# Optimization experiments

Hardware: AMD Instinct MI355X
Metric: run time of the kernel (lower is better)

The kernel has to match this reference:

```python
import jax, jax.numpy as jnp
import numpy as np

LAMBDA_TSA = 0.1
K = 25
P = 1
EPS = 1e-08
B, D = 16384, 16  # d == D required by the original math (Pz - Px)


def setup_inputs() -> dict:
    key = jax.random.key(0)
    k1, k2, k3, k4 = jax.random.split(key, 4)
    return {
        "outputs": jax.random.normal(k1, (B, D), dtype=jnp.float32),
        "targets": jax.random.normal(k2, (B, D), dtype=jnp.float32),
        "latent": jax.random.normal(k3, (B, D), dtype=jnp.float32),
        "raw": jax.random.normal(k4, (B, D), dtype=jnp.float32),
    }


def _tsa(raw, latent):
    # squared pairwise distances (monotone in cdist, so same top-k indices)
    sq = jnp.sum(raw * raw, axis=1)                      # [B]
    d2 = sq[:, None] + sq[None, :] - 2.0 * (raw @ raw.T)  # [B, B]
    _, idx = jax.lax.top_k(-d2, K + 1)                    # smallest K+1, ascending
    nbrs = idx[:, 1:]                                     # drop self -> [B, K]

    Z = latent[nbrs]                                      # [B, K, D]
    X = raw[nbrs]                                         # [B, K, D]
    Zc = Z - Z.mean(axis=1, keepdims=True)
    Xc = X - X.mean(axis=1, keepdims=True)
    denom = K - 1 + EPS
    Cz = jnp.einsum('bki,bkj->bij', Zc, Zc) / denom       # [B, D, D]
    Cx = jnp.einsum('bki,bkj->bij', Xc, Xc) / denom       # [B, D, D]

    _, Uz = jnp.linalg.eigh(Cz)                           # ascending eigenvalues
    _, Ux = jnp.linalg.eigh(Cx)
    Ui = Uz[:, :, -P:]                                    # top-P eigenvectors [B, D, P]
    Vi = Ux[:, :, -P:]
    Pz = jnp.einsum('bip,bjp->bij', Ui, Ui)               # tangent projectors [B, D, D]
    Px = jnp.einsum('bip,bjp->bij', Vi, Vi)
    return jnp.mean(jnp.sum((Pz - Px) ** 2, axis=(1, 2)))


def reference(outputs, targets, latent, raw):
    recon = jnp.mean((outputs - targets) ** 2)
    return recon + LAMBDA_TSA * _tsa(raw, latent)
```

## Files before the change

kernel.cpp:

```cpp
#include <hip/hip_runtime.h>
#include <cstdint>
#include <cstddef>

#define B_N   16384
#define D_DIM 16
#define K_NBR 25
#define SCAP  512
#define SMAXL 8
#define EPAD  20
#define PADR  20
#define NPART (B_N / 4)

#define WS_SQ_OFF   256
#define WS_RAWH_OFF (WS_SQ_OFF + 65536)
#define WS_RAWL_OFF (WS_RAWH_OFF + B_N * D_DIM * 2)
#define WS_LATH_OFF (WS_RAWL_OFF + B_N * D_DIM * 2)
#define WS_LATL_OFF (WS_LATH_OFF + B_N * D_DIM * 2)
#define WS_NBR_OFF  (WS_LATL_OFF + B_N * D_DIM * 2)
#define WS_PART_OFF (WS_NBR_OFF + B_N * K_NBR * 4)

typedef __attribute__((ext_vector_type(8))) short bf16x8;
typedef __attribute__((ext_vector_type(4))) float f32x4;
typedef __attribute__((ext_vector_type(4))) unsigned u32x4;

__device__ __forceinline__ unsigned short f2bf(float x) {
    unsigned u = __float_as_uint(x);
    unsigned r = (u + 0x7FFFu + ((u >> 16) & 1u)) >> 16;
    return (unsigned short)r;
}
__device__ __forceinline__ float bf2f(unsigned short h) {
    return __uint_as_float(((unsigned)h) << 16);
}
__device__ __forceinline__ unsigned med3u(unsigned a, unsigned b, unsigned c) {
    unsigned d;
    asm("v_med3_u32 %0, %1, %2, %3" : "=v"(d) : "v"(a), "v"(b), "v"(c));
    return d;
}

__global__ __launch_bounds__(256) void prep_kernel(const float4* __restrict__ rawv,
                                                   const float4* __restrict__ latv,
                                                   const float4* __restrict__ ov,
                                                   const float4* __restrict__ tv,
                                                   float* __restrict__ sqh,
                                                   unsigned short* __restrict__ rawh,
                                                   unsigned short* __restrict__ rawl,
                                                   unsigned short* __restrict__ lath,
                                                   unsigned short* __restrict__ latl,
                                                   float* __restrict__ accum) {
    int i = blockIdx.x * 256 + threadIdx.x;
    float v[16];
    {
        float4 r0 = rawv[i*4+0], r1 = rawv[i*4+1], r2 = rawv[i*4+2], r3 = rawv[i*4+3];
        v[0]=r0.x; v[1]=r0.y; v[2]=r0.z; v[3]=r0.w;
        v[4]=r1.x; v[5]=r1.y; v[6]=r1.z; v[7]=r1.w;
        v[8]=r2.x; v[9]=r2.y; v[10]=r2.z; v[11]=r2.w;
        v[12]=r3.x; v[13]=r3.y; v[14]=r3.z; v[15]=r3.w;
    }
    float s = 0.0f;
    unsigned short h[16], l[16];
    #pragma unroll
    for (int k = 0; k < 16; ++k) {
        s = fmaf(v[k], v[k], s);
        unsigned short hh = f2bf(v[k]);
        h[k] = hh;
        l[k] = f2bf(v[k] - bf2f(hh));
    }
    sqh[i] = 128.0f + 0.5f * s;
    #pragma unroll
    for (int q = 0; q < 4; ++q) {
        ((ushort4*)(rawh + (size_t)i*16))[q] = make_ushort4(h[q*4], h[q*4+1], h[q*4+2], h[q*4+3]);
        ((ushort4*)(rawl + (size_t)i*16))[q] = make_ushort4(l[q*4], l[q*4+1], l[q*4+2], l[q*4+3]);
    }
    {
        float4 r0 = latv[i*4+0], r1 = latv[i*4+1], r2 = latv[i*4+2], r3 = latv[i*4+3];
        v[0]=r0.x; v[1]=r0.y; v[2]=r0.z; v[3]=r0.w;
        v[4]=r1.x; v[5]=r1.y; v[6]=r1.z; v[7]=r1.w;
        v[8]=r2.x; v[9]=r2.y; v[10]=r2.z; v[11]=r2.w;
        v[12]=r3.x; v[13]=r3.y; v[14]=r3.z; v[15]=r3.w;
        #pragma unroll
        for (int k = 0; k < 16; ++k) {
            unsigned short hh = f2bf(v[k]);
            h[k] = hh;
            l[k] = f2bf(v[k] - bf2f(hh));
        }
        #pragma unroll
        for (int q = 0; q < 4; ++q) {
            ((ushort4*)(lath + (size_t)i*16))[q] = make_ushort4(h[q*4], h[q*4+1], h[q*4+2], h[q*4+3]);
            ((ushort4*)(latl + (size_t)i*16))[q] = make_ushort4(l[q*4], l[q*4+1], l[q*4+2], l[q*4+3]);
        }
    }

    float rs = 0.0f;
    #pragma unroll
    for (int q = 0; q < 4; ++q) {
        float4 o = ov[i*4+q], t = tv[i*4+q];
        float d;
        d = o.x - t.x; rs = fmaf(d, d, rs);
        d = o.y - t.y; rs = fmaf(d, d, rs);
        d = o.z - t.z; rs = fmaf(d, d, rs);
        d = o.w - t.w; rs = fmaf(d, d, rs);
    }
    #pragma unroll
    for (int off = 32; off >= 1; off >>= 1) rs += __shfl_down(rs, off, 64);
    if ((threadIdx.x & 63) == 0) atomicAdd(&accum[0], rs);
}

__global__ __launch_bounds__(1024) void scan_kernel(const unsigned short* __restrict__ rawh,
                                                    const unsigned short* __restrict__ rawl,
                                                    const float* __restrict__ sqh,
                                                    unsigned* __restrict__ nbrG) {
    __shared__ unsigned keyS[16 * SCAP];
    __shared__ int      nbrW[16][K_NBR];

    int tid  = threadIdx.x;
    int wave = tid >> 6;
    int lane = tid & 63;
    int quad = lane >> 4;
    int lnib = lane & 15;
    int i0   = blockIdx.x * 32;
    int koff = (quad & 1) * 8;

    const unsigned short* ab = (quad < 2 ? rawh : rawl) + (size_t)(i0 + lnib) * 16 + koff;
    bf16x8 afrag0, afrag1;
    {
        union { bf16x8 v; u32x4 u; } n0, n1;
        n0.v = *(const bf16x8*)ab;
        n1.v = *(const bf16x8*)(ab + 16 * 16);
        #pragma unroll
        for (int q = 0; q < 4; ++q) { n0.u[q] ^= 0x80008000u; n1.u[q] ^= 0x80008000u; }
        afrag0 = n0.v; afrag1 = n1.v;
    }

    unsigned s0[8], s1[8];
    #pragma unroll
    for (int r = 0; r < 8; ++r) { s0[r] = 0xFFFFFFFFu; s1[r] = 0xFFFFFFFFu; }

    for (int t = wave, m = 0; t < B_N / 16; t += 32, ++m) {
        int jA = t * 16 + lnib;
        int jB = jA + 256;
        bf16x8 bhA = *(const bf16x8*)(rawh + (size_t)jA * 16 + koff);
        bf16x8 blA = *(const bf16x8*)(rawl + (size_t)jA * 16 + koff);
        bf16x8 bhB = *(const bf16x8*)(rawh + (size_t)jB * 16 + koff);
        bf16x8 blB = *(const bf16x8*)(rawl + (size_t)jB * 16 + koff);
        float sqhA = sqh[jA];
        float sqhB = sqh[jB];
        unsigned cA = (unsigned)(m << 1);
        unsigned cB = cA | 1u;
        f32x4 a0A = {sqhA, sqhA, sqhA, sqhA}, a1A = {sqhA, sqhA, sqhA, sqhA};
        f32x4 a0B = {sqhB, sqhB, sqhB, sqhB}, a1B = {sqhB, sqhB, sqhB, sqhB};
        a0A = __builtin_amdgcn_mfma_f32_16x16x32_bf16(afrag0, blA, a0A, 0, 0, 0);
        a1A = __builtin_amdgcn_mfma_f32_16x16x32_bf16(afrag1, blA, a1A, 0, 0, 0);
        a0B = __builtin_amdgcn_mfma_f32_16x16x32_bf16(afrag0, blB, a0B, 0, 0, 0);
        a1B = __builtin_amdgcn_mfma_f32_16x16x32_bf16(afrag1, blB, a1B, 0, 0, 0);
        a0A = __builtin_amdgcn_mfma_f32_16x16x32_bf16(afrag0, bhA, a0A, 0, 0, 0);
        a1A = __builtin_amdgcn_mfma_f32_16x16x32_bf16(afrag1, bhA, a1A, 0, 0, 0);
        a0B = __builtin_amdgcn_mfma_f32_16x16x32_bf16(afrag0, bhB, a0B, 0, 0, 0);
        a1B = __builtin_amdgcn_mfma_f32_16x16x32_bf16(afrag1, bhB, a1B, 0, 0, 0);
        #pragma unroll
        for (int r = 0; r < 4; ++r) {
            unsigned key;
            key = (__float_as_uint(a0A[r]) & 0xFFFFFFC0u) | cA;
            s1[r] = med3u(s0[r], s1[r], key); s0[r] = min(s0[r], key);
            key = (__float_as_uint(a1A[r]) & 0xFFFFFFC0u) | cA;
            s1[4+r] = med3u(s0[4+r], s1[4+r], key); s0[4+r] = min(s0[4+r], key);
            key = (__float_as_uint(a0B[r]) & 0xFFFFFFC0u) | cB;
            s1[r] = med3u(s0[r], s1[r], key); s0[r] = min(s0[r], key);
            key = (__float_as_uint(a1B[r]) & 0xFFFFFFC0u) | cB;
            s1[4+r] = med3u(s0[4+r], s1[4+r], key); s0[4+r] = min(s0[4+r], key);
        }
    }

    unsigned long long ltm = (1ull << lane) - 1ull;
    for (int g = 0; g < 2; ++g) {
        __syncthreads();
        #pragma unroll
        for (int r = 0; r < 4; ++r) {
            int rloc = quad * 4 + r;
            int base = rloc * SCAP + wave * 32 + lnib * 2;
            keyS[base]     = s0[r + 4*g];
            keyS[base + 1] = s1[r + 4*g];
        }
        __syncthreads();

        int pt = i0 + g * 16 + wave;
        unsigned kl[SMAXL];
        #pragma unroll
        for (int tt = 0; tt < SMAXL; ++tt)
            kl[tt] = keyS[wave * SCAP + tt * 64 + lane];

        unsigned lo = 0x42000000u, hi = 0x44000000u;
        for (int it = 0; it < 32 && lo < hi; ++it) {
            unsigned mid = lo + ((hi - lo) >> 1);
            unsigned cc = 0;
            #pragma unroll
            for (int tt = 0; tt < SMAXL; ++tt)
                cc += (unsigned)__builtin_popcountll(__ballot(kl[tt] <= mid));
            if (cc >= K_NBR + 1) hi = mid; else lo = mid + 1;
        }
        unsigned T26 = hi;

        int base = 0;
        #pragma unroll
        for (int tt = 0; tt < SMAXL; ++tt) {
            unsigned kk = kl[tt];
            int wsrc = (tt << 1) | (lane >> 5);
            int ln2  = (lane >> 1) & 15;
            unsigned c = kk & 63u;
            int j = (wsrc << 4) | ((int)(c >> 1) << 9) | ((int)(c & 1u) << 8) | ln2;
            bool cnd = (kk <= T26) && (j != pt);
            unsigned long long mk = __ballot(cnd);
            if (cnd) {
                int pos = base + __builtin_popcountll(mk & ltm);
                if (pos < K_NBR) nbrW[wave][pos] = j;
            }
            base += __builtin_popcountll(mk);
        }
        if (lane == 0) {
            int got = base < K_NBR ? base : K_NBR;
            int pad = (got > 0) ? nbrW[wave][0] : pt;
            for (int q = got; q < K_NBR; ++q) nbrW[wave][q] = pad;
        }
        if (lane < K_NBR) nbrG[(size_t)pt * K_NBR + lane] = (unsigned)nbrW[wave][lane];
    }
}

__global__ __launch_bounds__(256) void eig_kernel(const unsigned short* __restrict__ lath,
                                                  const unsigned short* __restrict__ latl,
                                                  const unsigned short* __restrict__ rawh,
                                                  const unsigned short* __restrict__ rawl,
                                                  const unsigned* __restrict__ nbrG,
                                                  float* __restrict__ part) {
    __shared__ unsigned short MS[4][2][2][32 * EPAD];
    __shared__ __align__(16) unsigned CHp[4][2][16 * PADR];
    __shared__ float psum[4];

    int wave = threadIdx.x >> 6;
    int lane = threadIdx.x & 63;
    int quad = lane >> 4;
    int lnib = lane & 15;
    int pt   = blockIdx.x * 4 + wave;

    {
        int comm = lane >> 5;
        int row  = lane & 31;
        uint2* dh = (uint2*)&MS[wave][comm][0][row * EPAD];
        uint2* dl = (uint2*)&MS[wave][comm][1][row * EPAD];
        if (row < K_NBR) {
            int n = (int)nbrG[(size_t)pt * K_NBR + row];
            const uint2* sh = (const uint2*)((comm ? rawh : lath) + (size_t)n * 16);
            const uint2* sl = (const uint2*)((comm ? rawl : latl) + (size_t)n * 16);
            dh[0] = sh[0]; dh[1] = sh[1]; dh[2] = sh[2]; dh[3] = sh[3];
            dl[0] = sl[0]; dl[1] = sl[1]; dl[2] = sl[2]; dl[3] = sl[3];
        } else {
            uint2 z = make_uint2(0u, 0u);
            dh[0] = z; dh[1] = z; dh[2] = z; dh[3] = z;
            dl[0] = z; dl[1] = z; dl[2] = z; dl[3] = z;
        }
    }
    __syncthreads();

    bf16x8 ones;
    #pragma unroll
    for (int j = 0; j < 8; ++j) ones[j] = (short)0x3F80;

    const unsigned short* Mzh = &MS[wave][0][0][0];
    const unsigned short* Mzl = &MS[wave][0][1][0];
    const unsigned short* Mxh = &MS[wave][1][0][0];
    const unsigned short* Mxl = &MS[wave][1][1][0];

    bf16x8 fzh, fzl, fxh, fxl;
    #pragma unroll
    for (int j = 0; j < 8; ++j) {
        int k = quad * 8 + j;
        fzh[j] = (short)Mzh[k * EPAD + lnib];
        fzl[j] = (short)Mzl[k * EPAD + lnib];
        fxh[j] = (short)Mxh[k * EPAD + lnib];
        fxl[j] = (short)Mxl[k * EPAD + lnib];
    }

    f32x4 mz = {0.f,0.f,0.f,0.f}, mx = {0.f,0.f,0.f,0.f};
    mz = __builtin_amdgcn_mfma_f32_16x16x32_bf16(fzh, fzh, mz, 0, 0, 0);
    mx = __builtin_amdgcn_mfma_f32_16x16x32_bf16(fxh, fxh, mx, 0, 0, 0);
    mz = __builtin_amdgcn_mfma_f32_16x16x32_bf16(fzh, fzl, mz, 0, 0, 0);
    mx = __builtin_amdgcn_mfma_f32_16x16x32_bf16(fxh, fxl, mx, 0, 0, 0);
    mz = __builtin_amdgcn_mfma_f32_16x16x32_bf16(fzl, fzh, mz, 0, 0, 0);
    mx = __builtin_amdgcn_mfma_f32_16x16x32_bf16(fxl, fxh, mx, 0, 0, 0);
    f32x4 dz1 = {0.f,0.f,0.f,0.f}, dx1 = {0.f,0.f,0.f,0.f};
    dz1 = __builtin_amdgcn_mfma_f32_16x16x32_bf16(fzh, ones, dz1, 0, 0, 0);
    dx1 = __builtin_amdgcn_mfma_f32_16x16x32_bf16(fxh, ones, dx1, 0, 0, 0);
    dz1 = __builtin_amdgcn_mfma_f32_16x16x32_bf16(fzl, ones, dz1, 0, 0, 0);
    dx1 = __builtin_amdgcn_mfma_f32_16x16x32_bf16(fxl, ones, dx1, 0, 0, 0);
    f32x4 dz2 = {0.f,0.f,0.f,0.f}, dx2 = {0.f,0.f,0.f,0.f};
    dz2 = __builtin_amdgcn_mfma_f32_16x16x32_bf16(ones, fzh, dz2, 0, 0, 0);
    dx2 = __builtin_amdgcn_mfma_f32_16x16x32_bf16(ones, fxh, dx2, 0, 0, 0);
    dz2 = __builtin_amdgcn_mfma_f32_16x16x32_bf16(ones, fzl, dz2, 0, 0, 0);
    dx2 = __builtin_amdgcn_mfma_f32_16x16x32_bf16(ones, fxl, dx2, 0, 0, 0);

    f32x4 az, ax;
    #pragma unroll
    for (int r = 0; r < 4; ++r) {
        az[r] = mz[r] - dz1[r] * dz2[r] * 0.04f;
        ax[r] = mx[r] - dx1[r] * dx2[r] * 0.04f;
    }

    bool dg = (quad == (lnib >> 2));

    {
        float tz = dg ? az[lnib & 3] : 0.0f;
        float tx = dg ? ax[lnib & 3] : 0.0f;
        #pragma unroll
        for (int off = 1; off < 64; off <<= 1) {
            tz += __shfl_xor(tz, off, 64);
            tx += __shfl_xor(tx, off, 64);
        }
        float iz = 1.0f / fmaxf(tz, 1e-30f), ix = 1.0f / fmaxf(tx, 1e-30f);
        #pragma unroll
        for (int r = 0; r < 4; ++r) { az[r] *= iz; ax[r] *= ix; }
    }

    unsigned selF = (quad < 2) ? 0x05040100u : 0x07060302u;
    unsigned selG = (quad < 2) ? 0x07060302u : 0x05040100u;
    unsigned* Wz = &CHp[wave][0][0];
    unsigned* Wx = &CHp[wave][1][0];
    int wr = lnib * PADR + quad * 4;
    int rd = lnib * PADR + (quad & 1) * 8;

    for (int s = 0; s < 5; ++s) {
        u32x4 wz, wx;
        #pragma unroll
        for (int r = 0; r < 4; ++r) {
            unsigned u  = __float_as_uint(az[r]);
            unsigned h1 = u + 0x7FFFu + ((u >> 16) & 1u);
            float    rz = az[r] - __uint_as_float(h1 & 0xFFFF0000u);
            unsigned u2 = __float_as_uint(rz);
            unsigned h2 = u2 + 0x7FFFu + ((u2 >> 16) & 1u);
            wz[r] = __builtin_amdgcn_perm(h2, h1, 0x07060302u);
            u  = __float_as_uint(ax[r]);
            h1 = u + 0x7FFFu + ((u >> 16) & 1u);
            float rx = ax[r] - __uint_as_float(h1 & 0xFFFF0000u);
            u2 = __float_as_uint(rx);
            h2 = u2 + 0x7FFFu + ((u2 >> 16) & 1u);
            wx[r] = __builtin_amdgcn_perm(h2, h1, 0x07060302u);
        }
        *(u32x4*)&Wz[wr] = wz;
        *(u32x4*)&Wx[wr] = wx;
        u32x4 za = *(const u32x4*)&Wz[rd];
        u32x4 zb = *(const u32x4*)&Wz[rd + 4];
        u32x4 xa = *(const u32x4*)&Wx[rd];
        u32x4 xb = *(const u32x4*)&Wx[rd + 4];
        union { u32x4 u; bf16x8 v; } fz, gz, fx, gx;
        fz.u[0] = __builtin_amdgcn_perm(za[1], za[0], selF);
        fz.u[1] = __builtin_amdgcn_perm(za[3], za[2], selF);
        fz.u[2] = __builtin_amdgcn_perm(zb[1], zb[0], selF);
        fz.u[3] = __builtin_amdgcn_perm(zb[3], zb[2], selF);
        gz.u[0] = __builtin_amdgcn_perm(za[1], za[0], selG);
        gz.u[1] = __builtin_amdgcn_perm(za[3], za[2], selG);
        gz.u[2] = __builtin_amdgcn_perm(zb[1], zb[0], selG);
        gz.u[3] = __builtin_amdgcn_perm(zb[3], zb[2], selG);
        fx.u[0] = __builtin_amdgcn_perm(xa[1], xa[0], selF);
        fx.u[1] = __builtin_amdgcn_perm(xa[3], xa[2], selF);
        fx.u[2] = __builtin_amdgcn_perm(xb[1], xb[0], selF);
        fx.u[3] = __builtin_amdgcn_perm(xb[3], xb[2], selF);
        gx.u[0] = __builtin_amdgcn_perm(xa[1], xa[0], selG);
        gx.u[1] = __builtin_amdgcn_perm(xa[3], xa[2], selG);
        gx.u[2] = __builtin_amdgcn_perm(xb[1], xb[0], selG);
        gx.u[3] = __builtin_amdgcn_perm(xb[3], xb[2], selG);
        f32x4 nz = {0.f,0.f,0.f,0.f}, nx = {0.f,0.f,0.f,0.f};
        nz = __builtin_amdgcn_mfma_f32_16x16x32_bf16(fz.v, fz.v, nz, 0, 0, 0);
        nx = __builtin_amdgcn_mfma_f32_16x16x32_bf16(fx.v, fx.v, nx, 0, 0, 0);
        nz = __builtin_amdgcn_mfma_f32_16x16x32_bf16(fz.v, gz.v, nz, 0, 0, 0);
        nx = __builtin_amdgcn_mfma_f32_16x16x32_bf16(fx.v, gx.v, nx, 0, 0, 0);
        if (s == 2) {
            float tz = dg ? nz[lnib & 3] : 0.0f;
            float tx = dg ? nx[lnib & 3] : 0.0f;
            #pragma unroll
            for (int off = 1; off < 64; off <<= 1) {
                tz += __shfl_xor(tz, off, 64);
                tx += __shfl_xor(tx, off, 64);
            }
            float iz = 1.0f / fmaxf(tz, 1e-30f), ix = 1.0f / fmaxf(tx, 1e-30f);
            #pragma unroll
            for (int r = 0; r < 4; ++r) { az[r] = nz[r] * iz; ax[r] = nx[r] * ix; }
        } else {
            #pragma unroll
            for (int r = 0; r < 4; ++r) { az[r] = nz[r]; ax[r] = nx[r]; }
        }
    }

    float tz = dg ? az[lnib & 3] : 0.0f;
    float tx = dg ? ax[lnib & 3] : 0.0f;
    float dt = az[0]*ax[0] + az[1]*ax[1] + az[2]*ax[2] + az[3]*ax[3];
    #pragma unroll
    for (int off = 1; off < 64; off <<= 1) {
        tz += __shfl_xor(tz, off, 64);
        tx += __shfl_xor(tx, off, 64);
        dt += __shfl_xor(dt, off, 64);
    }
    if (lane == 0) psum[wave] = dt / fmaxf(tz * tx, 1e-30f);
    __syncthreads();
    if (threadIdx.x == 0)
        part[blockIdx.x] = psum[0] + psum[1] + psum[2] + psum[3];
}

__global__ __launch_bounds__(256) void final_kernel(const float* __restrict__ accum,
                                                    const float* __restrict__ part,
                                                    float* __restrict__ out) {
    __shared__ float ws[4];
    int tid = threadIdx.x;
    float s = 0.0f;
    for (int i = tid; i < NPART; i += 256) s += part[i];
    #pragma unroll
    for (int off = 32; off >= 1; off >>= 1) s += __shfl_down(s, off, 64);
    if ((tid & 63) == 0) ws[tid >> 6] = s;
    __syncthreads();
    if (tid == 0) {
        float dot2  = ws[0] + ws[1] + ws[2] + ws[3];
        float recon = accum[0] * (1.0f / (float)(B_N * D_DIM));
        float tsa   = 2.0f - 2.0f * (dot2 * (1.0f / (float)B_N));
        out[0] = recon + 0.1f * tsa;
    }
}

extern "C" void kernel_launch(void* const* d_in, const int* in_sizes, int n_in,
                              void* d_out, int out_size, void* d_ws, size_t ws_size,
                              hipStream_t stream) {
    const float* outputs = (const float*)d_in[0];
    const float* targets = (const float*)d_in[1];
    const float* latent  = (const float*)d_in[2];
    const float* raw     = (const float*)d_in[3];

    float* accum         = (float*)d_ws;
    float* sqh           = (float*)((char*)d_ws + WS_SQ_OFF);
    unsigned short* rawh = (unsigned short*)((char*)d_ws + WS_RAWH_OFF);
    unsigned short* rawl = (unsigned short*)((char*)d_ws + WS_RAWL_OFF);
    unsigned short* lath = (unsigned short*)((char*)d_ws + WS_LATH_OFF);
    unsigned short* latl = (unsigned short*)((char*)d_ws + WS_LATL_OFF);
    unsigned* nbrG       = (unsigned*)((char*)d_ws + WS_NBR_OFF);
    float* part          = (float*)((char*)d_ws + WS_PART_OFF);

    const float4* rawv = (const float4*)raw;
    const float4* latv = (const float4*)latent;

    hipMemsetAsync(d_ws, 0, 256, stream);
    prep_kernel<<<B_N / 256, 256, 0, stream>>>(rawv, latv, (const float4*)outputs,
                                               (const float4*)targets, sqh, rawh, rawl,
                                               lath, latl, accum);
    scan_kernel<<<B_N / 32, 1024, 0, stream>>>(rawh, rawl, sqh, nbrG);
    eig_kernel<<<B_N / 4, 256, 0, stream>>>(lath, latl, rawh, rawl, nbrG, part);
    final_kernel<<<1, 256, 0, stream>>>(accum, part, (float*)d_out);
}
```

Measured before the change: 169.9 us.

## Prefetch next scan tile and replace atomic recon sum with per-block partials

Result: slower. 186.2 us (+9.6%).

```diff
diff --git a/kernel.cpp b/kernel.cpp
--- a/kernel.cpp
+++ b/kernel.cpp
@@ -46,7 +46,8 @@
                                                    unsigned short* __restrict__ rawl,
                                                    unsigned short* __restrict__ lath,
                                                    unsigned short* __restrict__ latl,
-                                                   float* __restrict__ accum) {
+                                                   float* __restrict__ rblk) {
+    __shared__ float ws4[4];
     int i = blockIdx.x * 256 + threadIdx.x;
     float v[16];
     {
@@ -102,7 +103,9 @@
     }
     #pragma unroll
     for (int off = 32; off >= 1; off >>= 1) rs += __shfl_down(rs, off, 64);
-    if ((threadIdx.x & 63) == 0) atomicAdd(&accum[0], rs);
+    if ((threadIdx.x & 63) == 0) ws4[threadIdx.x >> 6] = rs;
+    __syncthreads();
+    if (threadIdx.x == 0) rblk[blockIdx.x] = ws4[0] + ws4[1] + ws4[2] + ws4[3];
 }
 
 __global__ __launch_bounds__(1024) void scan_kernel(const unsigned short* __restrict__ rawh,
@@ -135,15 +138,31 @@
     #pragma unroll
     for (int r = 0; r < 8; ++r) { s0[r] = 0xFFFFFFFFu; s1[r] = 0xFFFFFFFFu; }
 
-    for (int t = wave, m = 0; t < B_N / 16; t += 32, ++m) {
-        int jA = t * 16 + lnib;
-        int jB = jA + 256;
-        bf16x8 bhA = *(const bf16x8*)(rawh + (size_t)jA * 16 + koff);
-        bf16x8 blA = *(const bf16x8*)(rawl + (size_t)jA * 16 + koff);
-        bf16x8 bhB = *(const bf16x8*)(rawh + (size_t)jB * 16 + koff);
-        bf16x8 blB = *(const bf16x8*)(rawl + (size_t)jB * 16 + koff);
-        float sqhA = sqh[jA];
-        float sqhB = sqh[jB];
+    bf16x8 pbhA, pblA, pbhB, pblB;
+    float  psA, psB;
+    {
+        int ja = wave * 16 + lnib, jb = ja + 256;
+        pbhA = *(const bf16x8*)(rawh + (size_t)ja * 16 + koff);
+        pblA = *(const bf16x8*)(rawl + (size_t)ja * 16 + koff);
+        pbhB = *(const bf16x8*)(rawh + (size_t)jb * 16 + koff);
+        pblB = *(const bf16x8*)(rawl + (size_t)jb * 16 + koff);
+        psA = sqh[ja]; psB = sqh[jb];
+    }
+    int t = wave;
+    #pragma unroll 2
+    for (int m = 0; m < 32; ++m) {
+        bf16x8 bhA = pbhA, blA = pblA, bhB = pbhB, blB = pblB;
+        float sqhA = psA, sqhB = psB;
+        {
+            int tn = (m == 31) ? wave : (t + 32);
+            int ja = tn * 16 + lnib, jb = ja + 256;
+            pbhA = *(const bf16x8*)(rawh + (size_t)ja * 16 + koff);
+            pblA = *(const bf16x8*)(rawl + (size_t)ja * 16 + koff);
+            pbhB = *(const bf16x8*)(rawh + (size_t)jb * 16 + koff);
+            pblB = *(const bf16x8*)(rawl + (size_t)jb * 16 + koff);
+            psA = sqh[ja]; psB = sqh[jb];
+        }
+        t += 32;
         unsigned cA = (unsigned)(m << 1);
         unsigned cB = cA | 1u;
         f32x4 a0A = {sqhA, sqhA, sqhA, sqhA}, a1A = {sqhA, sqhA, sqhA, sqhA};
@@ -402,20 +421,24 @@
         part[blockIdx.x] = psum[0] + psum[1] + psum[2] + psum[3];
 }
 
-__global__ __launch_bounds__(256) void final_kernel(const float* __restrict__ accum,
+__global__ __launch_bounds__(256) void final_kernel(const float* __restrict__ rblk,
                                                     const float* __restrict__ part,
                                                     float* __restrict__ out) {
-    __shared__ float ws[4];
+    __shared__ float ws[8];
     int tid = threadIdx.x;
     float s = 0.0f;
     for (int i = tid; i < NPART; i += 256) s += part[i];
-    #pragma unroll
-    for (int off = 32; off >= 1; off >>= 1) s += __shfl_down(s, off, 64);
-    if ((tid & 63) == 0) ws[tid >> 6] = s;
+    float r = (tid < 64) ? rblk[tid] : 0.0f;
+    #pragma unroll
+    for (int off = 32; off >= 1; off >>= 1) {
+        s += __shfl_down(s, off, 64);
+        r += __shfl_down(r, off, 64);
+    }
+    if ((tid & 63) == 0) { ws[tid >> 6] = s; ws[4 + (tid >> 6)] = r; }
     __syncthreads();
     if (tid == 0) {
         float dot2  = ws[0] + ws[1] + ws[2] + ws[3];
-        float recon = accum[0] * (1.0f / (float)(B_N * D_DIM));
+        float recon = (ws[4] + ws[5] + ws[6] + ws[7]) * (1.0f / (float)(B_N * D_DIM));
         float tsa   = 2.0f - 2.0f * (dot2 * (1.0f / (float)B_N));
         out[0] = recon + 0.1f * tsa;
     }
@@ -429,7 +452,7 @@
     const float* latent  = (const float*)d_in[2];
     const float* raw     = (const float*)d_in[3];
 
-    float* accum         = (float*)d_ws;
+    float* rblk          = (float*)d_ws;
     float* sqh           = (float*)((char*)d_ws + WS_SQ_OFF);
     unsigned short* rawh = (unsigned short*)((char*)d_ws + WS_RAWH_OFF);
     unsigned short* rawl = (unsigned short*)((char*)d_ws + WS_RAWL_OFF);
@@ -441,11 +464,10 @@
     const float4* rawv = (const float4*)raw;
     const float4* latv = (const float4*)latent;
 
-    hipMemsetAsync(d_ws, 0, 256, stream);
     prep_kernel<<<B_N / 256, 256, 0, stream>>>(rawv, latv, (const float4*)outputs,
                                                (const float4*)targets, sqh, rawh, rawl,
-                                               lath, latl, accum);
+                                               lath, latl, rblk);
     scan_kernel<<<B_N / 32, 1024, 0, stream>>>(rawh, rawl, sqh, nbrG);
     eig_kernel<<<B_N / 4, 256, 0, stream>>>(lath, latl, rawh, rawl, nbrG, part);
-    final_kernel<<<1, 256, 0, stream>>>(accum, part, (float*)d_out);
-}
+    final_kernel<<<1, 256, 0, stream>>>(rblk, part, (float*)d_out);
+}
```
